# Optimization experiments

Measured on AMD Instinct MI355X. Metric: run time of the kernel, lower is better.

Reference implementation:

```python
import jax, jax.numpy as jnp
import numpy as np

N, E, IN, OUT, R, B = 50000, 800000, 16, 16, 90, 30


def setup_inputs() -> dict:
    key = jax.random.key(0)
    ks = jax.random.split(key, 9)
    h = jax.random.normal(ks[0], (N, IN), dtype=jnp.float32)
    he = jax.random.normal(ks[1], (E, IN), dtype=jnp.float32)
    Ws = jax.random.normal(ks[2], (OUT, IN), dtype=jnp.float32) * 0.1      # shared_weight.weight
    Wa = jax.random.normal(ks[3], (1, 3 * OUT), dtype=jnp.float32) * 0.1   # attn_fc.weight
    weight = jax.random.normal(ks[4], (B, IN, OUT), dtype=jnp.float32) * 0.1  # basis weights
    w_comp = jax.random.normal(ks[5], (R, B), dtype=jnp.float32) * 0.1        # basis coefficients
    src = jax.random.randint(ks[6], (E,), 0, N)
    dst = jax.random.randint(ks[7], (E,), 0, N)
    rel_type = jax.random.randint(ks[8], (E,), 0, R)
    return {"h": h, "he": he, "Ws": Ws, "Wa": Wa, "weight": weight,
            "w_comp": w_comp, "src": src, "dst": dst, "rel_type": rel_type}


def reference(h, he, Ws, Wa, weight, w_comp, src, dst, rel_type):
    n_nodes, in_dim = h.shape
    num_bases, _, out_dim = weight.shape
    num_rels = w_comp.shape[0]

    # Basis decomposition, replicating the original's reshape semantics exactly:
    # view [B,in,out] -> [in,B,out], matmul with w_comp [R,B] -> [in,R,out], view -> [R,in,out]
    V = weight.reshape(in_dim, num_bases, out_dim)
    W_rel = jnp.matmul(w_comp, V).reshape(num_rels, in_dim, out_dim)  # [R,in,out]

    # edge_attention: GAT-like score from concat(z_src, z_edge, z_dst)
    h_src = h[src]                      # [E,in]
    z_src = h_src @ Ws.T                # [E,out]
    z_dst = h[dst] @ Ws.T               # [E,out]
    z_e = he @ Ws.T                     # [E,out]
    e = jnp.concatenate([z_src, z_e, z_dst], axis=1) @ Wa.T  # [E,1] (no leaky_relu / no softmax in original)

    # message: per-edge relation-specific bmm, scaled by attention score
    msg = jnp.einsum('ei,eio->eo', h_src, W_rel[rel_type]) * e  # [E,out]

    # reduce: scatter-sum into destination nodes (bias=None, activation=None)
    h_out = jax.ops.segment_sum(msg, dst, num_segments=n_nodes)  # [N,out]
    return h_out
```

## Files before the change

### kernel.cpp

```cpp
#include <hip/hip_runtime.h>

#define N_NODES 50000
#define N_EDGES 800000
#define IN_DIM 16
#define OUT_DIM 16
#define N_RELS 90
#define N_BASES 30

#define CAP 24
#define LDS_STRIDE 260
#define EDGES_PER_BLK 3125

#define PREP_BLOCKS 91
#define DOTS_BLOCKS 196
#define ZERO_BLOCKS 196
#define HZ_BLOCKS 782

__device__ __forceinline__ float4 shfl_xor4(float4 v, int m) {
    float4 r;
    r.x = __shfl_xor(v.x, m); r.y = __shfl_xor(v.y, m);
    r.z = __shfl_xor(v.z, m); r.w = __shfl_xor(v.w, m);
    return r;
}

__global__ __launch_bounds__(256) void setup_kernel(
    const float* __restrict__ Ws,
    const float* __restrict__ Wa,
    const float* __restrict__ weight,
    const float* __restrict__ w_comp,
    const float* __restrict__ h,
    float* __restrict__ Wrel,
    float* __restrict__ avec,
    float2* __restrict__ s13,
    int* __restrict__ cnt,
    float* __restrict__ hout)
{
    int b = blockIdx.x;
    if (b < PREP_BLOCKS) {
        int f = b * 256 + threadIdx.x;
        if (f < N_RELS * IN_DIM * OUT_DIM) {
            int a   = f / (N_RELS * OUT_DIM);
            int rem = f % (N_RELS * OUT_DIM);
            int r   = rem / OUT_DIM;
            int o   = rem % OUT_DIM;
            float acc = 0.f;
            #pragma unroll
            for (int bb = 0; bb < N_BASES; ++bb)
                acc += w_comp[r * N_BASES + bb] * weight[a * (N_BASES * OUT_DIM) + bb * OUT_DIM + o];
            Wrel[f] = acc;
        } else if (f < N_RELS * IN_DIM * OUT_DIM + 48) {
            int g = f - N_RELS * IN_DIM * OUT_DIM;
            int k = g / IN_DIM;
            int i = g % IN_DIM;
            float acc = 0.f;
            #pragma unroll
            for (int o = 0; o < OUT_DIM; ++o)
                acc += Wa[k * OUT_DIM + o] * Ws[o * IN_DIM + i];
            avec[g] = acc;
        }
    } else if (b < PREP_BLOCKS + DOTS_BLOCKS) {
        __shared__ float la[48];
        if (threadIdx.x < 48) {
            int k = threadIdx.x / IN_DIM;
            int i = threadIdx.x % IN_DIM;
            float acc = 0.f;
            #pragma unroll
            for (int o = 0; o < OUT_DIM; ++o)
                acc += Wa[k * OUT_DIM + o] * Ws[o * IN_DIM + i];
            la[threadIdx.x] = acc;
        }
        __syncthreads();
        int n = (b - PREP_BLOCKS) * 256 + threadIdx.x;
        if (n >= N_NODES) return;
        const float4* p = (const float4*)(h + (size_t)n * IN_DIM);
        float d1 = 0.f, d3 = 0.f;
        #pragma unroll
        for (int i = 0; i < 4; ++i) {
            float4 v = p[i];
            d1 += v.x * la[4*i+0] + v.y * la[4*i+1] + v.z * la[4*i+2] + v.w * la[4*i+3];
            d3 += v.x * la[32+4*i+0] + v.y * la[32+4*i+1] + v.z * la[32+4*i+2] + v.w * la[32+4*i+3];
        }
        s13[n] = make_float2(d1, d3);
    } else if (b < PREP_BLOCKS + DOTS_BLOCKS + ZERO_BLOCKS) {
        int n = (b - PREP_BLOCKS - DOTS_BLOCKS) * 256 + threadIdx.x;
        if (n < N_NODES) cnt[n] = 0;
    } else {
        int idx = (b - PREP_BLOCKS - DOTS_BLOCKS - ZERO_BLOCKS) * 256 + threadIdx.x;
        if (idx < N_NODES * OUT_DIM / 4) {
            float4 z = {0.f, 0.f, 0.f, 0.f};
            ((float4*)hout)[idx] = z;
        }
    }
}

__global__ __launch_bounds__(1024) void compute_lds_kernel(
    const float* __restrict__ h,
    const float* __restrict__ he,
    const int* __restrict__ src,
    const int* __restrict__ dst,
    const int* __restrict__ rel,
    const float* __restrict__ Wrel,
    const float* __restrict__ avec,
    const float2* __restrict__ s13,
    int* __restrict__ cnt,
    float* __restrict__ bucket,
    float* __restrict__ hout)
{
    extern __shared__ float lw[];

    for (int j = threadIdx.x; j < N_RELS * 64; j += 1024) {
        int r = j >> 6;
        int w = j & 63;
        float4 v = ((const float4*)Wrel)[r * 64 + w];
        *(float4*)(lw + r * LDS_STRIDE + w * 4) = v;
    }
    __syncthreads();

    const int t = threadIdx.x;
    const int q = t & 3;
    const int grp = t >> 2;
    const int lbase = (t & 63) & ~3;
    const int ebeg = blockIdx.x * EDGES_PER_BLK;
    const int eend = ebeg + EDGES_PER_BLK;

    float4 av = *(const float4*)(avec + 16 + 4 * q);

    for (int base = ebeg + grp; base < eend; base += 1024) {
        int e[4], s[4], d[4], r[4];
        bool val[4];

        #pragma unroll
        for (int k = 0; k < 4; ++k) {
            e[k] = base + k * 256;
            val[k] = (e[k] < eend);
            int ec = val[k] ? e[k] : ebeg;
            s[k] = src[ec]; d[k] = dst[ec]; r[k] = rel[ec];
        }

        float4 heq[4], hq[4];
        float2 svs[4], svd[4];
        #pragma unroll
        for (int k = 0; k < 4; ++k) {
            int ec = val[k] ? e[k] : ebeg;
            heq[k] = *(const float4*)(he + (size_t)ec * IN_DIM + q * 4);
            hq[k]  = *(const float4*)(h  + (size_t)s[k] * IN_DIM + q * 4);
            svs[k] = s13[s[k]];
            svd[k] = s13[d[k]];
        }

        int slot[4];
        #pragma unroll
        for (int k = 0; k < 4; ++k) {
            slot[k] = 0;
            if (q == 0 && val[k]) slot[k] = atomicAdd(&cnt[d[k]], 1);
        }

        #pragma unroll
        for (int k = 0; k < 4; ++k) {
            if (!val[k]) continue;
            int sl = __shfl(slot[k], lbase);

            float pd = heq[k].x * av.x + heq[k].y * av.y + heq[k].z * av.z + heq[k].w * av.w;
            pd += __shfl_xor(pd, 1);
            pd += __shfl_xor(pd, 2);
            float score = svs[k].x + svd[k].y + pd;

            float4 o1 = shfl_xor4(hq[k], 1);
            float4 o2 = shfl_xor4(hq[k], 2);
            float4 o3 = shfl_xor4(o1, 2);
            bool q0 = (q == 0), q1 = (q == 1), q2 = (q == 2);
            float4 row0 = q0 ? hq[k] : q1 ? o1 : q2 ? o2 : o3;
            float4 row1 = q0 ? o1 : q1 ? hq[k] : q2 ? o3 : o2;
            float4 row2 = q0 ? o2 : q1 ? o3 : q2 ? hq[k] : o1;
            float4 row3 = q0 ? o3 : q1 ? o2 : q2 ? o1 : hq[k];
            float hs[16] = {row0.x,row0.y,row0.z,row0.w, row1.x,row1.y,row1.z,row1.w,
                            row2.x,row2.y,row2.z,row2.w, row3.x,row3.y,row3.z,row3.w};

            const float* wb = lw + (size_t)r[k] * LDS_STRIDE + q * 4;
            float4 acc = {0.f, 0.f, 0.f, 0.f};
            #pragma unroll
            for (int i = 0; i < 16; ++i) {
                float4 w = *(const float4*)(wb + i * 16);
                float hv = hs[i];
                acc.x += hv * w.x; acc.y += hv * w.y; acc.z += hv * w.z; acc.w += hv * w.w;
            }
            acc.x *= score; acc.y *= score; acc.z *= score; acc.w *= score;

            if (sl < CAP) {
                *(float4*)(bucket + ((size_t)d[k] * CAP + sl) * OUT_DIM + q * 4) = acc;
            } else {
                float* outp = hout + (size_t)d[k] * OUT_DIM + q * 4;
                atomicAdd(outp + 0, acc.x);
                atomicAdd(outp + 1, acc.y);
                atomicAdd(outp + 2, acc.z);
                atomicAdd(outp + 3, acc.w);
            }
        }
    }
}

__global__ __launch_bounds__(256) void reduce_bucket_kernel(
    const float* __restrict__ bucket,
    const int* __restrict__ cnt,
    float* __restrict__ hout)
{
    int tid = blockIdx.x * 256 + threadIdx.x;
    int n = tid >> 4;
    int l = tid & 15;
    int q = l & 3;
    int p = l >> 2;
    if (n >= N_NODES) return;

    int deg = cnt[n];
    int m = deg > CAP ? CAP : deg;
    const float4* bp = (const float4*)(bucket + (size_t)n * CAP * OUT_DIM) + q;
    float4 acc = {0.f, 0.f, 0.f, 0.f};
    for (int j = p; j < m; j += 4) {
        float4 v = bp[j * 4];
        acc.x += v.x; acc.y += v.y; acc.z += v.z; acc.w += v.w;
    }
    acc.x += __shfl_xor(acc.x, 4); acc.y += __shfl_xor(acc.y, 4);
    acc.z += __shfl_xor(acc.z, 4); acc.w += __shfl_xor(acc.w, 4);
    acc.x += __shfl_xor(acc.x, 8); acc.y += __shfl_xor(acc.y, 8);
    acc.z += __shfl_xor(acc.z, 8); acc.w += __shfl_xor(acc.w, 8);

    if (p == 0) {
        if (deg <= CAP) {
            *(float4*)(hout + (size_t)n * OUT_DIM + q * 4) = acc;
        } else {
            float* outp = hout + (size_t)n * OUT_DIM + q * 4;
            atomicAdd(outp + 0, acc.x);
            atomicAdd(outp + 1, acc.y);
            atomicAdd(outp + 2, acc.z);
            atomicAdd(outp + 3, acc.w);
        }
    }
}

__global__ __launch_bounds__(256) void prep_kernel(
    const float* __restrict__ Ws, const float* __restrict__ Wa,
    const float* __restrict__ weight, const float* __restrict__ w_comp,
    float* __restrict__ Wrel, float* __restrict__ avec)
{
    int f = blockIdx.x * blockDim.x + threadIdx.x;
    if (f < N_RELS * IN_DIM * OUT_DIM) {
        int a   = f / (N_RELS * OUT_DIM);
        int rem = f % (N_RELS * OUT_DIM);
        int r   = rem / OUT_DIM;
        int o   = rem % OUT_DIM;
        float acc = 0.f;
        #pragma unroll
        for (int b = 0; b < N_BASES; ++b)
            acc += w_comp[r * N_BASES + b] * weight[a * (N_BASES * OUT_DIM) + b * OUT_DIM + o];
        Wrel[f] = acc;
    } else if (f < N_RELS * IN_DIM * OUT_DIM + 48) {
        int g = f - N_RELS * IN_DIM * OUT_DIM;
        int k = g / IN_DIM;
        int i = g % IN_DIM;
        float acc = 0.f;
        #pragma unroll
        for (int o = 0; o < OUT_DIM; ++o)
            acc += Wa[k * OUT_DIM + o] * Ws[o * IN_DIM + i];
        avec[g] = acc;
    }
}

__global__ __launch_bounds__(256) void edge_atomic_kernel(
    const float* __restrict__ h,
    const float* __restrict__ he,
    const int* __restrict__ src,
    const int* __restrict__ dst,
    const int* __restrict__ rel,
    const float* __restrict__ Wrel,
    const float* __restrict__ avec,
    float* __restrict__ hout)
{
    int e = blockIdx.x * blockDim.x + threadIdx.x;
    if (e >= N_EDGES) return;
    int s = src[e], d = dst[e], r = rel[e];
    float hs[IN_DIM];
    const float4* p = (const float4*)(h + (size_t)s * IN_DIM);
    #pragma unroll
    for (int i = 0; i < 4; ++i) {
        float4 v = p[i];
        hs[4*i+0] = v.x; hs[4*i+1] = v.y; hs[4*i+2] = v.z; hs[4*i+3] = v.w;
    }
    float score = 0.f;
    #pragma unroll
    for (int i = 0; i < IN_DIM; ++i) score += hs[i] * avec[i];
    const float4* qe = (const float4*)(he + (size_t)e * IN_DIM);
    #pragma unroll
    for (int i = 0; i < 4; ++i) {
        float4 v = qe[i];
        score += v.x * avec[16+4*i] + v.y * avec[17+4*i] + v.z * avec[18+4*i] + v.w * avec[19+4*i];
    }
    const float4* pd = (const float4*)(h + (size_t)d * IN_DIM);
    #pragma unroll
    for (int i = 0; i < 4; ++i) {
        float4 v = pd[i];
        score += v.x * avec[32+4*i] + v.y * avec[33+4*i] + v.z * avec[34+4*i] + v.w * avec[35+4*i];
    }
    float acc[OUT_DIM];
    #pragma unroll
    for (int o = 0; o < OUT_DIM; ++o) acc[o] = 0.f;
    const float* W = Wrel + (size_t)r * 256;
    #pragma unroll
    for (int i = 0; i < IN_DIM; ++i) {
        float hv = hs[i];
        #pragma unroll
        for (int o = 0; o < OUT_DIM; ++o) acc[o] += hv * W[i * OUT_DIM + o];
    }
    float* outp = hout + (size_t)d * OUT_DIM;
    #pragma unroll
    for (int o = 0; o < OUT_DIM; ++o) atomicAdd(outp + o, acc[o] * score);
}

extern "C" void kernel_launch(void* const* d_in, const int* in_sizes, int n_in,
                              void* d_out, int out_size, void* d_ws, size_t ws_size,
                              hipStream_t stream) {
    const float* h      = (const float*)d_in[0];
    const float* he     = (const float*)d_in[1];
    const float* Ws     = (const float*)d_in[2];
    const float* Wa     = (const float*)d_in[3];
    const float* weight = (const float*)d_in[4];
    const float* w_comp = (const float*)d_in[5];
    const int*   src    = (const int*)d_in[6];
    const int*   dst    = (const int*)d_in[7];
    const int*   rel    = (const int*)d_in[8];
    float* hout = (float*)d_out;

    const size_t OFF_WREL   = 0;
    const size_t OFF_AVEC   = 23040;
    const size_t OFF_S13    = 23104;
    const size_t OFF_CNT    = 123104;
    const size_t OFF_BUCKET = 173104;
    const size_t NEED_BUCKET = (OFF_BUCKET + (size_t)N_NODES * CAP * OUT_DIM) * 4;

    float* wsf  = (float*)d_ws;
    float* Wrel = wsf + OFF_WREL;
    float* avec = wsf + OFF_AVEC;
    float2* s13 = (float2*)(wsf + OFF_S13);
    int* cnt    = (int*)(wsf + OFF_CNT);

    if (ws_size >= NEED_BUCKET) {
        float* bucket = wsf + OFF_BUCKET;

        setup_kernel<<<PREP_BLOCKS + DOTS_BLOCKS + ZERO_BLOCKS + HZ_BLOCKS, 256, 0, stream>>>(
            Ws, Wa, weight, w_comp, h, Wrel, avec, s13, cnt, hout);
        compute_lds_kernel<<<N_EDGES / EDGES_PER_BLK, 1024,
                             N_RELS * LDS_STRIDE * sizeof(float), stream>>>(
            h, he, src, dst, rel, Wrel, avec, s13, cnt, bucket, hout);
        reduce_bucket_kernel<<<(N_NODES * 16 + 255) / 256, 256, 0, stream>>>(
            bucket, cnt, hout);
    } else {
        hipMemsetAsync(d_out, 0, (size_t)out_size * sizeof(float), stream);
        int total = N_RELS * IN_DIM * OUT_DIM + 48;
        prep_kernel<<<(total + 255) / 256, 256, 0, stream>>>(Ws, Wa, weight, w_comp, Wrel, avec);
        edge_atomic_kernel<<<(N_EDGES + 255) / 256, 256, 0, stream>>>(
            h, he, src, dst, rel, Wrel, avec, hout);
    }
}
```

Baseline: 188.6 us.

## Store relation weights and edge message buckets in bf16, shrink edge blocks

The per-relation weight matrices are now kept as bf16 in global memory and LDS, and the per-edge messages written to the bucket buffer are packed as bf16, with widening back to fp32 in the compute and reduce kernels. This halves the bucket write and read traffic and the LDS footprint, which allows more resident blocks. Edges per block drop from 3125 to 1600, giving twice as many blocks. The cost is lost precision in both the weights and the partial messages, which may exceed tolerance, plus extra conversion ALU work.

```diff
diff --git a/kernel.cpp b/kernel.cpp
--- a/kernel.cpp
+++ b/kernel.cpp
@@ -8,13 +8,16 @@
 #define N_BASES 30
 
 #define CAP 24
-#define LDS_STRIDE 260
-#define EDGES_PER_BLK 3125
+#define LDS_USTRIDE 264
+#define EDGES_PER_BLK 1600
 
 #define PREP_BLOCKS 91
 #define DOTS_BLOCKS 196
 #define ZERO_BLOCKS 196
 #define HZ_BLOCKS 782
+
+typedef unsigned int uint32;
+typedef unsigned short ushort16;
 
 __device__ __forceinline__ float4 shfl_xor4(float4 v, int m) {
     float4 r;
@@ -22,6 +25,14 @@
     r.z = __shfl_xor(v.z, m); r.w = __shfl_xor(v.w, m);
     return r;
 }
+
+__device__ __forceinline__ ushort16 f2bf(float f) {
+    uint32 b = __float_as_uint(f);
+    b = (b + 0x7FFFu + ((b >> 16) & 1u)) >> 16;
+    return (ushort16)b;
+}
+__device__ __forceinline__ float bflo(uint32 u) { return __uint_as_float(u << 16); }
+__device__ __forceinline__ float bfhi(uint32 u) { return __uint_as_float(u & 0xffff0000u); }
 
 __global__ __launch_bounds__(256) void setup_kernel(
     const float* __restrict__ Ws,
@@ -29,7 +40,7 @@
     const float* __restrict__ weight,
     const float* __restrict__ w_comp,
     const float* __restrict__ h,
-    float* __restrict__ Wrel,
+    ushort16* __restrict__ Wrelh,
     float* __restrict__ avec,
     float2* __restrict__ s13,
     int* __restrict__ cnt,
@@ -47,7 +58,7 @@
             #pragma unroll
             for (int bb = 0; bb < N_BASES; ++bb)
                 acc += w_comp[r * N_BASES + bb] * weight[a * (N_BASES * OUT_DIM) + bb * OUT_DIM + o];
-            Wrel[f] = acc;
+            Wrelh[f] = f2bf(acc);
         } else if (f < N_RELS * IN_DIM * OUT_DIM + 48) {
             int g = f - N_RELS * IN_DIM * OUT_DIM;
             int k = g / IN_DIM;
@@ -99,20 +110,20 @@
     const int* __restrict__ src,
     const int* __restrict__ dst,
     const int* __restrict__ rel,
-    const float* __restrict__ Wrel,
+    const ushort16* __restrict__ Wrelh,
     const float* __restrict__ avec,
     const float2* __restrict__ s13,
     int* __restrict__ cnt,
-    float* __restrict__ bucket,
+    ushort16* __restrict__ bucket,
     float* __restrict__ hout)
 {
-    extern __shared__ float lw[];
-
-    for (int j = threadIdx.x; j < N_RELS * 64; j += 1024) {
-        int r = j >> 6;
-        int w = j & 63;
-        float4 v = ((const float4*)Wrel)[r * 64 + w];
-        *(float4*)(lw + r * LDS_STRIDE + w * 4) = v;
+    extern __shared__ uint32 lwu[];
+
+    const uint32* Wu = (const uint32*)Wrelh;
+    for (int j = threadIdx.x; j < N_RELS * 128; j += 1024) {
+        int r = j >> 7;
+        int w = j & 127;
+        lwu[r * (LDS_USTRIDE / 2) + w] = Wu[j];
     }
     __syncthreads();
 
@@ -176,18 +187,23 @@
             float hs[16] = {row0.x,row0.y,row0.z,row0.w, row1.x,row1.y,row1.z,row1.w,
                             row2.x,row2.y,row2.z,row2.w, row3.x,row3.y,row3.z,row3.w};
 
-            const float* wb = lw + (size_t)r[k] * LDS_STRIDE + q * 4;
+            const uint32* wb = lwu + (size_t)r[k] * (LDS_USTRIDE / 2) + q * 2;
             float4 acc = {0.f, 0.f, 0.f, 0.f};
             #pragma unroll
             for (int i = 0; i < 16; ++i) {
-                float4 w = *(const float4*)(wb + i * 16);
+                uint32 u0 = wb[i * 8 + 0];
+                uint32 u1 = wb[i * 8 + 1];
                 float hv = hs[i];
-                acc.x += hv * w.x; acc.y += hv * w.y; acc.z += hv * w.z; acc.w += hv * w.w;
+                acc.x += hv * bflo(u0); acc.y += hv * bfhi(u0);
+                acc.z += hv * bflo(u1); acc.w += hv * bfhi(u1);
             }
             acc.x *= score; acc.y *= score; acc.z *= score; acc.w *= score;
 
             if (sl < CAP) {
-                *(float4*)(bucket + ((size_t)d[k] * CAP + sl) * OUT_DIM + q * 4) = acc;
+                uint32 p0 = ((uint32)f2bf(acc.y) << 16) | (uint32)f2bf(acc.x);
+                uint32 p1 = ((uint32)f2bf(acc.w) << 16) | (uint32)f2bf(acc.z);
+                uint2 pkt = make_uint2(p0, p1);
+                *(uint2*)((ushort16*)bucket + ((size_t)d[k] * CAP + sl) * OUT_DIM + q * 4) = pkt;
             } else {
                 float* outp = hout + (size_t)d[k] * OUT_DIM + q * 4;
                 atomicAdd(outp + 0, acc.x);
@@ -200,7 +216,7 @@
 }
 
 __global__ __launch_bounds__(256) void reduce_bucket_kernel(
-    const float* __restrict__ bucket,
+    const ushort16* __restrict__ bucket,
     const int* __restrict__ cnt,
     float* __restrict__ hout)
 {
@@ -213,11 +229,11 @@
 
     int deg = cnt[n];
     int m = deg > CAP ? CAP : deg;
-    const float4* bp = (const float4*)(bucket + (size_t)n * CAP * OUT_DIM) + q;
     float4 acc = {0.f, 0.f, 0.f, 0.f};
     for (int j = p; j < m; j += 4) {
-        float4 v = bp[j * 4];
-        acc.x += v.x; acc.y += v.y; acc.z += v.z; acc.w += v.w;
+        const uint2 v = *(const uint2*)(bucket + ((size_t)n * CAP + j) * OUT_DIM + q * 4);
+        acc.x += bflo(v.x); acc.y += bfhi(v.x);
+        acc.z += bflo(v.y); acc.w += bfhi(v.y);
     }
     acc.x += __shfl_xor(acc.x, 4); acc.y += __shfl_xor(acc.y, 4);
     acc.z += __shfl_xor(acc.z, 4); acc.w += __shfl_xor(acc.w, 4);
@@ -329,34 +345,36 @@
     const int*   rel    = (const int*)d_in[8];
     float* hout = (float*)d_out;
 
-    const size_t OFF_WREL   = 0;
-    const size_t OFF_AVEC   = 23040;
-    const size_t OFF_S13    = 23104;
-    const size_t OFF_CNT    = 123104;
-    const size_t OFF_BUCKET = 173104;
-    const size_t NEED_BUCKET = (OFF_BUCKET + (size_t)N_NODES * CAP * OUT_DIM) * 4;
+    const size_t OFF_WRELH  = 0;
+    const size_t OFF_AVEC   = 11520;
+    const size_t OFF_S13    = 11584;
+    const size_t OFF_CNT    = 111584;
+    const size_t OFF_BUCKET = 161584;
+    const size_t NEED_BUCKET = (OFF_BUCKET + (size_t)N_NODES * CAP * OUT_DIM / 2) * 4;
 
     float* wsf  = (float*)d_ws;
-    float* Wrel = wsf + OFF_WREL;
+    ushort16* Wrelh = (ushort16*)(wsf + OFF_WRELH);
     float* avec = wsf + OFF_AVEC;
     float2* s13 = (float2*)(wsf + OFF_S13);
     int* cnt    = (int*)(wsf + OFF_CNT);
 
     if (ws_size >= NEED_BUCKET) {
-        float* bucket = wsf + OFF_BUCKET;
+        ushort16* bucket = (ushort16*)(wsf + OFF_BUCKET);
 
         setup_kernel<<<PREP_BLOCKS + DOTS_BLOCKS + ZERO_BLOCKS + HZ_BLOCKS, 256, 0, stream>>>(
-            Ws, Wa, weight, w_comp, h, Wrel, avec, s13, cnt, hout);
+            Ws, Wa, weight, w_comp, h, Wrelh, avec, s13, cnt, hout);
         compute_lds_kernel<<<N_EDGES / EDGES_PER_BLK, 1024,
-                             N_RELS * LDS_STRIDE * sizeof(float), stream>>>(
-            h, he, src, dst, rel, Wrel, avec, s13, cnt, bucket, hout);
+                             N_RELS * (LDS_USTRIDE / 2) * sizeof(uint32), stream>>>(
+            h, he, src, dst, rel, Wrelh, avec, s13, cnt, bucket, hout);
         reduce_bucket_kernel<<<(N_NODES * 16 + 255) / 256, 256, 0, stream>>>(
             bucket, cnt, hout);
     } else {
         hipMemsetAsync(d_out, 0, (size_t)out_size * sizeof(float), stream);
+        float* Wrel = wsf;
+        float* avf  = wsf + 23040;
         int total = N_RELS * IN_DIM * OUT_DIM + 48;
-        prep_kernel<<<(total + 255) / 256, 256, 0, stream>>>(Ws, Wa, weight, w_comp, Wrel, avec);
+        prep_kernel<<<(total + 255) / 256, 256, 0, stream>>>(Ws, Wa, weight, w_comp, Wrel, avf);
         edge_atomic_kernel<<<(N_EDGES + 255) / 256, 256, 0, stream>>>(
-            h, he, src, dst, rel, Wrel, avec, hout);
-    }
-}
+            h, he, src, dst, rel, Wrel, avf, hout);
+    }
+}
```

New measurement: 191.1 us. About the same (+1.3%).
